# Performance work log

Hardware: AMD Instinct MI355X
Metric: run time of the kernel (lower is better)

## Reference

```python
import jax, jax.numpy as jnp
import numpy as np

B, S, D, DK = 4, 2048, 1024, 1024


def setup_inputs() -> dict:
    key = jax.random.key(0)
    kx, kq, kk, kv = jax.random.split(key, 4)
    return {
        "x": jax.random.normal(kx, (B, S, D), dtype=jnp.float32),
        "WQ": jax.random.normal(kq, (D, DK), dtype=jnp.float32),
        "WK": jax.random.normal(kk, (D, DK), dtype=jnp.float32),
        "WV": jax.random.normal(kv, (D, DK), dtype=jnp.float32),
    }


def reference(x, WQ, WK, WV):
    # q,k,v: [B,S,DK]
    q = x @ WQ
    k = x @ WK
    v = x @ WV
    scale = 1.0 / np.sqrt(DK).astype(np.float32)
    scores = jnp.einsum("bqd,bkd->bqk", q, k) * scale  # [B,S,S]
    # NOTE: original uses nn.Softmax(dim=1) -> normalize over the QUERY axis (axis 1)
    attn = jax.nn.softmax(scores, axis=1)
    return jnp.einsum("bqk,bkd->bqd", attn, v)
```

## Files before the change

kernel.cpp:

```cpp
#include <hip/hip_runtime.h>

constexpr int Bc  = 4;
constexpr int Sc  = 2048;
constexpr int Dc  = 1024;
constexpr int DKc = 1024;
constexpr long BSc = (long)Bc * Sc;

typedef __attribute__((ext_vector_type(8))) __bf16 bf16x8;
typedef __attribute__((ext_vector_type(4))) __bf16 bf16x4;
typedef __attribute__((ext_vector_type(4))) float  floatx4;

__device__ inline __bf16 f2bf(float f) {
  unsigned u = __builtin_bit_cast(unsigned, f);
  u = (u + 0x7FFFu + ((u >> 16) & 1u)) >> 16;
  unsigned short s = (unsigned short)u;
  return __builtin_bit_cast(__bf16, s);
}
__device__ inline float bf2f(__bf16 h) {
  unsigned u = ((unsigned)__builtin_bit_cast(unsigned short, h)) << 16;
  return __builtin_bit_cast(float, u);
}

__device__ inline void stage16(const __bf16* g, __bf16* l) {
  __builtin_amdgcn_global_load_lds(
      (const __attribute__((address_space(1))) unsigned int*)g,
      (__attribute__((address_space(3))) unsigned int*)l, 16, 0, 0);
}

__device__ __forceinline__ void bar_raw() {
  asm volatile("" ::: "memory");
  __builtin_amdgcn_s_barrier();
  asm volatile("" ::: "memory");
}
template <int N>
__device__ __forceinline__ void vmwait() {
  asm volatile("s_waitcnt vmcnt(%0)" :: "n"(N));
  __builtin_amdgcn_sched_barrier(0);
}

__global__ __launch_bounds__(256) void prep(
    const float* __restrict__ x,  __bf16* __restrict__ xhi, __bf16* __restrict__ xlo,
    const float* __restrict__ wq, __bf16* __restrict__ qhi, __bf16* __restrict__ qlo,
    const float* __restrict__ wk, __bf16* __restrict__ khi, __bf16* __restrict__ klo,
    const float* __restrict__ wv, __bf16* __restrict__ vthi) {
  __shared__ float tile[32][33];
  long blk = blockIdx.x;
  if (blk >= 10240) {
    int t   = (int)(blk - 10240);
    int bx  = t & 31, by = t >> 5;
    int thx = threadIdx.x & 31, thy = threadIdx.x >> 5;
    int xI  = bx * 32 + thx, yI = by * 32 + thy;
#pragma unroll
    for (int j = 0; j < 32; j += 8)
      tile[thy + j][thx] = wv[(long)(yI + j) * DKc + xI];
    __syncthreads();
    int xO = by * 32 + thx, yO = bx * 32 + thy;
#pragma unroll
    for (int j = 0; j < 32; j += 8)
      vthi[(long)(yO + j) * Dc + xO] = f2bf(tile[thx][thy + j]);
    return;
  }
  const float* in; __bf16 *hi, *lo; long base;
  if (blk < 8192)      { in = x;  hi = xhi; lo = xlo; base = blk * 1024; }
  else if (blk < 9216) { in = wq; hi = qhi; lo = qlo; base = (blk - 8192) * 1024; }
  else                 { in = wk; hi = khi; lo = klo; base = (blk - 9216) * 1024; }
  long i = base + (long)threadIdx.x * 4;
  float4 f = *(const float4*)(in + i);
  __bf16 h0 = f2bf(f.x), h1 = f2bf(f.y), h2 = f2bf(f.z), h3 = f2bf(f.w);
  bf16x4 hv = {h0, h1, h2, h3};
  bf16x4 lv = {f2bf(f.x - bf2f(h0)), f2bf(f.y - bf2f(h1)),
               f2bf(f.z - bf2f(h2)), f2bf(f.w - bf2f(h3))};
  *(bf16x4*)(hi + i) = hv;
  *(bf16x4*)(lo + i) = lv;
}

struct SCtx {
  const __bf16 *pAh, *pAl, *pBh, *pBl;
  __bf16* lds;
  int stLds;
  int aoff, boff;
};

template <int W, bool SAL, bool S2A, bool S2B>
__device__ __forceinline__ void tile_step(const SCtx& c, int t,
                                          floatx4 (&acc)[8][4]) {
  constexpr int K = 1024;
  constexpr int BH = 8192, BL = 16384, AL = 24576;
  __bf16* cur = c.lds + (t & 1) * 32768;
  __bf16* oth = c.lds + ((t & 1) ^ 1) * 32768;
  bf16x8 af[8], bfr[4], bfl[4];

  vmwait<W>();
  bar_raw();
  if (SAL) {
    const __bf16* s = c.pAl + (t + 1) * 32;
    stage16(s, oth + AL + c.stLds);
    stage16(s + 16 * K, oth + AL + c.stLds + 512);
  }
#pragma unroll
  for (int mt = 0; mt < 8; ++mt)
    af[mt] = *(const bf16x8*)(cur + c.aoff + mt * 512);
#pragma unroll
  for (int nt = 0; nt < 4; ++nt)
    bfr[nt] = *(const bf16x8*)(cur + BH + c.boff + nt * 512);
#pragma unroll
  for (int nt = 0; nt < 4; ++nt)
    bfl[nt] = *(const bf16x8*)(cur + BL + c.boff + nt * 512);

  __builtin_amdgcn_s_setprio(1);
#pragma unroll
  for (int mt = 0; mt < 8; ++mt)
#pragma unroll
    for (int nt = 0; nt < 4; ++nt)
      acc[mt][nt] = __builtin_amdgcn_mfma_f32_16x16x32_bf16(af[mt], bfr[nt], acc[mt][nt], 0, 0, 0);
#pragma unroll
  for (int mt = 0; mt < 8; ++mt)
#pragma unroll
    for (int nt = 0; nt < 4; ++nt)
      acc[mt][nt] = __builtin_amdgcn_mfma_f32_16x16x32_bf16(af[mt], bfl[nt], acc[mt][nt], 0, 0, 0);
  __builtin_amdgcn_s_setprio(0);

  bar_raw();
  if (S2A) {
    const __bf16* sa = c.pAh + (t + 2) * 32;
    stage16(sa, cur + c.stLds);
    stage16(sa + 16 * K, cur + c.stLds + 512);
    stage16(c.pBh + (t + 2) * 32, cur + BH + c.stLds);
  }
  if (S2B) {
    stage16(c.pBh + (t + 2) * 32 + 16 * K, cur + BH + c.stLds + 512);
    const __bf16* sb = c.pBl + (t + 2) * 32;
    stage16(sb, cur + BL + c.stLds);
    stage16(sb + 16 * K, cur + BL + c.stLds + 512);
  }
  {
    bf16x8 afl[8];
#pragma unroll
    for (int mt = 0; mt < 8; ++mt)
      afl[mt] = *(const bf16x8*)(cur + AL + c.aoff + mt * 512);
    __builtin_amdgcn_s_setprio(1);
#pragma unroll
    for (int mt = 0; mt < 8; ++mt)
#pragma unroll
      for (int nt = 0; nt < 4; ++nt)
        acc[mt][nt] = __builtin_amdgcn_mfma_f32_16x16x32_bf16(afl[mt], bfr[nt], acc[mt][nt], 0, 0, 0);
    __builtin_amdgcn_s_setprio(0);
  }
}

__global__ __launch_bounds__(512, 2) void gemm_s5(
    const __bf16* __restrict__ thi, const __bf16* __restrict__ tlo,
    const __bf16* __restrict__ xhi, const __bf16* __restrict__ xlo,
    __bf16* __restrict__ P, float* __restrict__ Pmax, float* __restrict__ Psum) {
  __shared__ __align__(16) __bf16 smem[65536];
  constexpr int K = 1024;
  const int b    = blockIdx.z;
  const int m0   = blockIdx.y * 256;
  const int n0   = blockIdx.x * 256;
  const int wave = threadIdx.x >> 6;
  const int lane = threadIdx.x & 63;
  const int wm   = wave >> 2;
  const int wn   = wave & 3;
  const int sr   = lane >> 2;
  const int scol = ((lane & 3) ^ ((sr >> 1) & 3)) * 8;
  const int frow = lane & 15;
  const int pko  = ((lane >> 4) ^ ((frow >> 1) & 3)) * 8;

  SCtx c;
  const long batch = (long)Sc * 1024;
  const long ar = (long)(m0 + wave * 32 + sr) * K + scol;
  const long br = (long)(n0 + wave * 32 + sr) * K + scol;
  c.pAh = thi + (long)b * batch + ar;
  c.pAl = tlo + (long)b * batch + ar;
  c.pBh = xhi + (long)b * batch + br;
  c.pBl = xlo + (long)b * batch + br;
  c.lds = smem;
  c.stLds = wave * 1024;
  c.aoff = (wm * 128 + frow) * 32 + pko;
  c.boff = (wn * 64 + frow) * 32 + pko;

  {
    __bf16* b0 = smem;
    __bf16* b1 = smem + 32768;
    stage16(c.pAh, b0 + c.stLds);               stage16(c.pAh + 16 * K, b0 + c.stLds + 512);
    stage16(c.pBh, b0 + 8192 + c.stLds);        stage16(c.pBh + 16 * K, b0 + 8192 + c.stLds + 512);
    stage16(c.pBl, b0 + 16384 + c.stLds);       stage16(c.pBl + 16 * K, b0 + 16384 + c.stLds + 512);
    stage16(c.pAl, b0 + 24576 + c.stLds);       stage16(c.pAl + 16 * K, b0 + 24576 + c.stLds + 512);
    stage16(c.pAh + 32, b1 + c.stLds);          stage16(c.pAh + 32 + 16 * K, b1 + c.stLds + 512);
    stage16(c.pBh + 32, b1 + 8192 + c.stLds);   stage16(c.pBh + 32 + 16 * K, b1 + 8192 + c.stLds + 512);
    stage16(c.pBl + 32, b1 + 16384 + c.stLds);  stage16(c.pBl + 32 + 16 * K, b1 + 16384 + c.stLds + 512);
  }

  floatx4 acc[8][4];
  const floatx4 zero = {0.f, 0.f, 0.f, 0.f};
#pragma unroll
  for (int i = 0; i < 8; ++i)
#pragma unroll
    for (int j = 0; j < 4; ++j) acc[i][j] = zero;

#pragma unroll 1
  for (int t = 0; t < 30; ++t) tile_step<6, true, true, true>(c, t, acc);
  tile_step<6, true, false, false>(c, 30, acc);
  tile_step<0, false, false, false>(c, 31, acc);

  const int crow0 = (lane >> 4) * 4;
  const int ccol  = lane & 15;
  const int tid   = threadIdx.x;
  constexpr float scale = 0.03125f;
  float* smax = (float*)smem;
  float* ssum = smax + 512;

  float cm[4];
#pragma unroll
  for (int nt = 0; nt < 4; ++nt) {
    float mx = -3.0e38f;
#pragma unroll
    for (int mt = 0; mt < 8; ++mt)
#pragma unroll
      for (int r = 0; r < 4; ++r) mx = fmaxf(mx, acc[mt][nt][r] * scale);
    cm[nt] = mx;
  }
#pragma unroll
  for (int off = 16; off <= 32; off <<= 1)
#pragma unroll
    for (int nt = 0; nt < 4; ++nt)
      cm[nt] = fmaxf(cm[nt], __shfl_xor(cm[nt], off, 64));
  __syncthreads();
  if (lane < 16)
#pragma unroll
    for (int nt = 0; nt < 4; ++nt)
      smax[wm * 256 + wn * 64 + nt * 16 + lane] = cm[nt];
  __syncthreads();
  float mfin[4];
#pragma unroll
  for (int nt = 0; nt < 4; ++nt) {
    int cidx = wn * 64 + nt * 16 + ccol;
    mfin[nt] = fmaxf(smax[cidx], smax[256 + cidx]);
  }
  float ps[4];
#pragma unroll
  for (int nt = 0; nt < 4; ++nt) {
    float s = 0.f;
#pragma unroll
    for (int mt = 0; mt < 8; ++mt)
#pragma unroll
      for (int r = 0; r < 4; ++r)
        s += __expf(acc[mt][nt][r] * scale - mfin[nt]);
    ps[nt] = s;
  }
#pragma unroll
  for (int off = 16; off <= 32; off <<= 1)
#pragma unroll
    for (int nt = 0; nt < 4; ++nt) ps[nt] += __shfl_xor(ps[nt], off, 64);
  if (lane < 16)
#pragma unroll
    for (int nt = 0; nt < 4; ++nt)
      ssum[wm * 256 + wn * 64 + nt * 16 + lane] = ps[nt];
  __syncthreads();
  if (tid < 256) {
    long o = ((long)b * 8 + blockIdx.y) * Sc + n0 + tid;
    Pmax[o] = fmaxf(smax[tid], smax[256 + tid]);
    Psum[o] = ssum[tid] + ssum[256 + tid];
  }
  __syncthreads();
  __bf16* sT = smem;
#pragma unroll
  for (int nt = 0; nt < 4; ++nt) {
    int col = wn * 64 + nt * 16 + ccol;
#pragma unroll
    for (int mt = 0; mt < 8; ++mt) {
      int rowb = wm * 128 + mt * 16 + crow0;
#pragma unroll
      for (int r = 0; r < 4; ++r) {
        int row = rowb + r;
        sT[row * 256 + (col ^ (((row >> 2) & 3) << 4))] =
            f2bf(__expf(acc[mt][nt][r] * scale - mfin[nt]));
      }
    }
  }
  __syncthreads();
  __bf16* Pb = P + (long)b * ((long)Sc * Sc);
#pragma unroll
  for (int cc = 0; cc < 16; ++cc) {
    int flat = cc * 4096 + tid * 8;
    int row = flat >> 8, col = flat & 255;
    *(bf16x8*)(Pb + (long)(m0 + row) * Sc + n0 + col) =
        *(const bf16x8*)(sT + row * 256 + (col ^ (((row >> 2) & 3) << 4)));
  }
}

struct TCtx {
  const __bf16 *pAh, *pAl, *pBh, *pBl;
  __bf16* lds;
  int stA, stB;
  int aoff, boff;
};

template <int W, bool SAL, bool S2AB, bool S2B>
__device__ __forceinline__ void tile_step_t(const TCtx& c, int t,
                                            floatx4 (&acc)[4][4]) {
  constexpr int K = 1024;
  constexpr int BH = 8192, BL = 12288, AL = 16384, BUF = 24576;
  __bf16* cur = c.lds + (t & 1) * BUF;
  __bf16* oth = c.lds + ((t & 1) ^ 1) * BUF;
  bf16x8 af[4], bfr[4], bfl[4], afl[4];

  vmwait<W>();
  bar_raw();
  if (SAL) {
    const __bf16* s = c.pAl + (t + 1) * 32;
    stage16(s, oth + AL + c.stA);
    stage16(s + 16 * K, oth + AL + c.stA + 512);
  }
#pragma unroll
  for (int mt = 0; mt < 4; ++mt)
    af[mt] = *(const bf16x8*)(cur + c.aoff + mt * 512);
#pragma unroll
  for (int nt = 0; nt < 4; ++nt)
    bfr[nt] = *(const bf16x8*)(cur + BH + c.boff + nt * 512);
#pragma unroll
  for (int nt = 0; nt < 4; ++nt)
    bfl[nt] = *(const bf16x8*)(cur + BL + c.boff + nt * 512);
#pragma unroll
  for (int mt = 0; mt < 4; ++mt)
    afl[mt] = *(const bf16x8*)(cur + AL + c.aoff + mt * 512);

  __builtin_amdgcn_s_setprio(1);
#pragma unroll
  for (int mt = 0; mt < 4; ++mt)
#pragma unroll
    for (int nt = 0; nt < 4; ++nt)
      acc[mt][nt] = __builtin_amdgcn_mfma_f32_16x16x32_bf16(af[mt], bfr[nt], acc[mt][nt], 0, 0, 0);
#pragma unroll
  for (int mt = 0; mt < 4; ++mt)
#pragma unroll
    for (int nt = 0; nt < 4; ++nt)
      acc[mt][nt] = __builtin_amdgcn_mfma_f32_16x16x32_bf16(af[mt], bfl[nt], acc[mt][nt], 0, 0, 0);
#pragma unroll
  for (int mt = 0; mt < 4; ++mt)
#pragma unroll
    for (int nt = 0; nt < 4; ++nt)
      acc[mt][nt] = __builtin_amdgcn_mfma_f32_16x16x32_bf16(afl[mt], bfr[nt], acc[mt][nt], 0, 0, 0);
  __builtin_amdgcn_s_setprio(0);

  bar_raw();
  if (S2AB) {
    const __bf16* sa = c.pAh + (t + 2) * 32;
    stage16(sa, cur + c.stA);
    stage16(sa + 16 * K, cur + c.stA + 512);
    stage16(c.pBh + (t + 2) * 32, cur + BH + c.stB);
  }
  if (S2B) stage16(c.pBl + (t + 2) * 32, cur + BL + c.stB);
}

__global__ __launch_bounds__(512, 2) void gemm_t5(
    const __bf16* __restrict__ xhi, const __bf16* __restrict__ xlo,
    const __bf16* __restrict__ gthi, const __bf16* __restrict__ gtlo,
    __bf16* __restrict__ thi, __bf16* __restrict__ tlo) {
  __shared__ __align__(16) __bf16 smem[49152];
  constexpr int K = 1024;
  const int m0   = blockIdx.y * 256;
  const int n0   = blockIdx.x * 128;
  const int wave = threadIdx.x >> 6;
  const int lane = threadIdx.x & 63;
  const int wm   = wave >> 1;
  const int wn   = wave & 1;
  const int sr   = lane >> 2;
  const int scol = ((lane & 3) ^ ((sr >> 1) & 3)) * 8;
  const int frow = lane & 15;
  const int pko  = ((lane >> 4) ^ ((frow >> 1) & 3)) * 8;

  TCtx c;
  const long ar = (long)(m0 + wave * 32 + sr) * K + scol;
  const long br = (long)(n0 + wave * 16 + sr) * K + scol;
  c.pAh = xhi + ar;
  c.pAl = xlo + ar;
  c.pBh = gthi + br;
  c.pBl = gtlo + br;
  c.lds = smem;
  c.stA = wave * 1024;
  c.stB = wave * 512;
  c.aoff = (wm * 64 + frow) * 32 + pko;
  c.boff = (wn * 64 + frow) * 32 + pko;

  {
    __bf16* b0 = smem;
    __bf16* b1 = smem + 24576;
    stage16(c.pAh, b0 + c.stA);          stage16(c.pAh + 16 * K, b0 + c.stA + 512);
    stage16(c.pBh, b0 + 8192 + c.stB);
    stage16(c.pBl, b0 + 12288 + c.stB);
    stage16(c.pAl, b0 + 16384 + c.stA);  stage16(c.pAl + 16 * K, b0 + 16384 + c.stA + 512);
    stage16(c.pAh + 32, b1 + c.stA);     stage16(c.pAh + 32 + 16 * K, b1 + c.stA + 512);
    stage16(c.pBh + 32, b1 + 8192 + c.stB);
    stage16(c.pBl + 32, b1 + 12288 + c.stB);
  }

  floatx4 acc[4][4];
  const floatx4 zero = {0.f, 0.f, 0.f, 0.f};
#pragma unroll
  for (int i = 0; i < 4; ++i)
#pragma unroll
    for (int j = 0; j < 4; ++j) acc[i][j] = zero;

#pragma unroll 1
  for (int t = 0; t < 30; ++t) tile_step_t<4, true, true, true>(c, t, acc);
  tile_step_t<4, true, false, false>(c, 30, acc);
  tile_step_t<0, false, false, false>(c, 31, acc);

  const int crow0 = (lane >> 4) * 4;
  const int ccol  = lane & 15;
  const int tid   = threadIdx.x;
  __bf16* sT = smem;
#pragma unroll 1
  for (int pass = 0; pass < 2; ++pass) {
    __syncthreads();
#pragma unroll
    for (int nt = 0; nt < 4; ++nt) {
      int col = wn * 64 + nt * 16 + ccol;
#pragma unroll
      for (int mt = 0; mt < 4; ++mt) {
        int rowb = wm * 64 + mt * 16 + crow0;
#pragma unroll
        for (int r = 0; r < 4; ++r) {
          int row = rowb + r;
          float v = acc[mt][nt][r];
          __bf16 h = f2bf(v);
          sT[row * 128 + (col ^ (((row >> 2) & 3) << 4))] =
              pass ? f2bf(v - bf2f(h)) : h;
        }
      }
    }
    __syncthreads();
    __bf16* dst = pass ? tlo : thi;
#pragma unroll
    for (int cc = 0; cc < 8; ++cc) {
      int flat = cc * 4096 + tid * 8;
      int row = flat >> 7, col = flat & 127;
      *(bf16x8*)(dst + (long)(m0 + row) * DKc + n0 + col) =
          *(const bf16x8*)(sT + row * 128 + (col ^ (((row >> 2) & 3) << 4)));
    }
  }
}

struct PCtx {
  const __bf16 *pA, *pB;
  int stA, stB;
  int aoff, boff;
};

template <int KK, int W, bool STG>
__device__ __forceinline__ void tile_step_pv(const PCtx& c, int t,
                                             __bf16* cur, __bf16* dst,
                                             floatx4 (&acc)[4][4]) {
  vmwait<W>();
  bar_raw();
  if (STG) {
    const __bf16* a = c.pA + (t + 2) * 64;
    stage16(a, dst + c.stA);
    stage16(a + 16 * KK, dst + c.stA + 512);
    stage16(c.pB + (t + 2) * 64, dst + 16384 + c.stB);
    stage16(a + 32, dst + 8192 + c.stA);
    stage16(a + 32 + 16 * KK, dst + 8192 + c.stA + 512);
    stage16(c.pB + (t + 2) * 64 + 32, dst + 20480 + c.stB);
  }
  bf16x8 a0[4], b0[4], a1[4], b1[4];
#pragma unroll
  for (int mt = 0; mt < 4; ++mt)
    a0[mt] = *(const bf16x8*)(cur + c.aoff + mt * 512);
#pragma unroll
  for (int nt = 0; nt < 4; ++nt)
    b0[nt] = *(const bf16x8*)(cur + 16384 + c.boff + nt * 512);
#pragma unroll
  for (int mt = 0; mt < 4; ++mt)
    a1[mt] = *(const bf16x8*)(cur + 8192 + c.aoff + mt * 512);
#pragma unroll
  for (int nt = 0; nt < 4; ++nt)
    b1[nt] = *(const bf16x8*)(cur + 20480 + c.boff + nt * 512);
  __builtin_amdgcn_s_setprio(1);
#pragma unroll
  for (int mt = 0; mt < 4; ++mt)
#pragma unroll
    for (int nt = 0; nt < 4; ++nt)
      acc[mt][nt] = __builtin_amdgcn_mfma_f32_16x16x32_bf16(a0[mt], b0[nt], acc[mt][nt], 0, 0, 0);
#pragma unroll
  for (int mt = 0; mt < 4; ++mt)
#pragma unroll
    for (int nt = 0; nt < 4; ++nt)
      acc[mt][nt] = __builtin_amdgcn_mfma_f32_16x16x32_bf16(a1[mt], b1[nt], acc[mt][nt], 0, 0, 0);
  __builtin_amdgcn_s_setprio(0);
}

__global__ __launch_bounds__(256) void scale_p(__bf16* __restrict__ P,
                                               const float* __restrict__ ffac) {
  long i8 = (long)blockIdx.x * 256 + threadIdx.x;
  long base = i8 * 8;
  int k = (int)(base & (Sc - 1));
  int q = (int)((base >> 11) & (Sc - 1));
  int b = (int)(base >> 22);
  int t = q >> 8;
  const float* f = ffac + (((long)b * 8 + t) << 11) + k;
  float4 f0 = *(const float4*)f;
  float4 f1 = *(const float4*)(f + 4);
  bf16x8 p = *(const bf16x8*)(P + base);
  bf16x8 o;
  o[0] = f2bf(bf2f(p[0]) * f0.x);
  o[1] = f2bf(bf2f(p[1]) * f0.y);
  o[2] = f2bf(bf2f(p[2]) * f0.z);
  o[3] = f2bf(bf2f(p[3]) * f0.w);
  o[4] = f2bf(bf2f(p[4]) * f1.x);
  o[5] = f2bf(bf2f(p[5]) * f1.y);
  o[6] = f2bf(bf2f(p[6]) * f1.z);
  o[7] = f2bf(bf2f(p[7]) * f1.w);
  *(bf16x8*)(P + base) = o;
}

__global__ __launch_bounds__(512, 2) void gemm_pv4(
    const __bf16* __restrict__ P, const __bf16* __restrict__ vt,
    float* __restrict__ out) {
  __shared__ __align__(16) __bf16 smem[73728];
  constexpr int K = 2048;
  const int b    = blockIdx.z;
  const int m0   = blockIdx.x * 256;
  const int n0   = blockIdx.y * 128;
  const int wave = threadIdx.x >> 6;
  const int lane = threadIdx.x & 63;
  const int wm   = wave >> 1;
  const int wn   = wave & 1;
  const int sr   = lane >> 2;
  const int scol = ((lane & 3) ^ ((sr >> 1) & 3)) * 8;
  const int frow = lane & 15;
  const int pko  = ((lane >> 4) ^ ((frow >> 1) & 3)) * 8;

  PCtx c;
  c.pA = P + (long)b * Sc * Sc + (long)(m0 + wave * 32 + sr) * K + scol;
  c.pB = vt + (long)b * DKc * Sc + (long)(n0 + wave * 16 + sr) * K + scol;
  c.stA = wave * 1024;
  c.stB = wave * 512;
  c.aoff = (wm * 64 + frow) * 32 + pko;
  c.boff = (wn * 64 + frow) * 32 + pko;

  __bf16* B0 = smem;
  __bf16* B1 = smem + 24576;
  __bf16* B2 = smem + 49152;

  stage16(c.pA, B0 + c.stA);            stage16(c.pA + 16 * K, B0 + c.stA + 512);
  stage16(c.pB, B0 + 16384 + c.stB);
  stage16(c.pA + 32, B0 + 8192 + c.stA); stage16(c.pA + 32 + 16 * K, B0 + 8192 + c.stA + 512);
  stage16(c.pB + 32, B0 + 20480 + c.stB);
  stage16(c.pA + 64, B1 + c.stA);       stage16(c.pA + 64 + 16 * K, B1 + c.stA + 512);
  stage16(c.pB + 64, B1 + 16384 + c.stB);
  stage16(c.pA + 96, B1 + 8192 + c.stA); stage16(c.pA + 96 + 16 * K, B1 + 8192 + c.stA + 512);
  stage16(c.pB + 96, B1 + 20480 + c.stB);

  floatx4 acc[4][4];
  const floatx4 zero = {0.f, 0.f, 0.f, 0.f};
#pragma unroll
  for (int i = 0; i < 4; ++i)
#pragma unroll
    for (int j = 0; j < 4; ++j) acc[i][j] = zero;

#pragma unroll 1
  for (int t = 0; t < 30; t += 3) {
    tile_step_pv<2048, 6, true>(c, t,     B0, B2, acc);
    tile_step_pv<2048, 6, true>(c, t + 1, B1, B0, acc);
    tile_step_pv<2048, 6, true>(c, t + 2, B2, B1, acc);
  }
  tile_step_pv<2048, 6, false>(c, 30, B0, B0, acc);
  tile_step_pv<2048, 0, false>(c, 31, B1, B1, acc);

  const int crow0 = (lane >> 4) * 4;
  const int ccol  = lane & 15;
#pragma unroll
  for (int nt = 0; nt < 4; ++nt) {
    int cn = n0 + wn * 64 + nt * 16 + ccol;
#pragma unroll
    for (int mt = 0; mt < 4; ++mt) {
#pragma unroll
      for (int r = 0; r < 4; ++r) {
        int cm_ = m0 + wm * 64 + mt * 16 + crow0 + r;
        out[(long)b * Sc * DKc + (long)cm_ * DKc + cn] = acc[mt][nt][r];
      }
    }
  }
}

constexpr int VSTR2 = 264;

__global__ __launch_bounds__(512, 2) void gemm_v4(
    const __bf16* __restrict__ xhi, const __bf16* __restrict__ wvthi,
    __bf16* __restrict__ vt) {
  __shared__ __align__(16) __bf16 smem[73728];
  constexpr int K = 1024;
  const int m0   = blockIdx.y * 256;
  const int n0   = blockIdx.x * 128;
  const int wave = threadIdx.x >> 6;
  const int lane = threadIdx.x & 63;
  const int wm   = wave >> 1;
  const int wn   = wave & 1;
  const int sr   = lane >> 2;
  const int scol = ((lane & 3) ^ ((sr >> 1) & 3)) * 8;
  const int frow = lane & 15;
  const int pko  = ((lane >> 4) ^ ((frow >> 1) & 3)) * 8;

  PCtx c;
  c.pA = xhi + (long)(m0 + wave * 32 + sr) * K + scol;
  c.pB = wvthi + (long)(n0 + wave * 16 + sr) * K + scol;
  c.stA = wave * 1024;
  c.stB = wave * 512;
  c.aoff = (wm * 64 + frow) * 32 + pko;
  c.boff = (wn * 64 + frow) * 32 + pko;

  __bf16* B0 = smem;
  __bf16* B1 = smem + 24576;
  __bf16* B2 = smem + 49152;

  stage16(c.pA, B0 + c.stA);            stage16(c.pA + 16 * K, B0 + c.stA + 512);
  stage16(c.pB, B0 + 16384 + c.stB);
  stage16(c.pA + 32, B0 + 8192 + c.stA); stage16(c.pA + 32 + 16 * K, B0 + 8192 + c.stA + 512);
  stage16(c.pB + 32, B0 + 20480 + c.stB);
  stage16(c.pA + 64, B1 + c.stA);       stage16(c.pA + 64 + 16 * K, B1 + c.stA + 512);
  stage16(c.pB + 64, B1 + 16384 + c.stB);
  stage16(c.pA + 96, B1 + 8192 + c.stA); stage16(c.pA + 96 + 16 * K, B1 + 8192 + c.stA + 512);
  stage16(c.pB + 96, B1 + 20480 + c.stB);

  floatx4 acc[4][4];
  const floatx4 zero = {0.f, 0.f, 0.f, 0.f};
#pragma unroll
  for (int i = 0; i < 4; ++i)
#pragma unroll
    for (int j = 0; j < 4; ++j) acc[i][j] = zero;

#pragma unroll 1
  for (int t = 0; t < 12; t += 3) {
    tile_step_pv<1024, 6, true>(c, t,     B0, B2, acc);
    tile_step_pv<1024, 6, true>(c, t + 1, B1, B0, acc);
    tile_step_pv<1024, 6, true>(c, t + 2, B2, B1, acc);
  }
  tile_step_pv<1024, 6, true >(c, 12, B0, B2, acc);
  tile_step_pv<1024, 6, true >(c, 13, B1, B0, acc);
  tile_step_pv<1024, 6, false>(c, 14, B2, B2, acc);
  tile_step_pv<1024, 0, false>(c, 15, B0, B0, acc);

  const int crow0 = (lane >> 4) * 4;
  const int ccol  = lane & 15;
  const int tid   = threadIdx.x;
  __syncthreads();
  __bf16* sT = smem;
#pragma unroll
  for (int nt = 0; nt < 4; ++nt) {
    int nl = wn * 64 + nt * 16 + ccol;
#pragma unroll
    for (int mt = 0; mt < 4; ++mt) {
      int ml = wm * 64 + mt * 16 + crow0;
#pragma unroll
      for (int r = 0; r < 4; ++r)
        sT[(long)nl * VSTR2 + ml + r] = f2bf(acc[mt][nt][r]);
    }
  }
  __syncthreads();
  const int bb   = m0 >> 11;
  const int seq0 = m0 & (Sc - 1);
  __bf16* dst = vt + (long)bb * DKc * Sc + seq0;
#pragma unroll
  for (int cc = 0; cc < 8; ++cc) {
    int flat = cc * 4096 + tid * 8;
    int row = flat >> 8, col = flat & 255;
    *(bf16x8*)(dst + (long)(n0 + row) * Sc + col) =
        *(const bf16x8*)(sT + (long)row * VSTR2 + col);
  }
}

__global__ __launch_bounds__(256) void gemm_g64(
    const __bf16* __restrict__ Ahi, const __bf16* __restrict__ Alo,
    const __bf16* __restrict__ Bhi, const __bf16* __restrict__ Blo,
    __bf16* __restrict__ Chi, __bf16* __restrict__ Clo) {
  constexpr int K = Dc, N = DKc;
  __shared__ __align__(16) char smem[16384];
  __bf16* sAh = (__bf16*)smem;
  __bf16* sBh = sAh + 64 * 32;
  __bf16* sAl = sBh + 64 * 32;
  __bf16* sBl = sAl + 64 * 32;

  const int wave = threadIdx.x >> 6;
  const int lane = threadIdx.x & 63;
  const int wm   = wave >> 1, wn = wave & 1;
  const int m0   = blockIdx.y * 64;
  const int n0   = blockIdx.x * 64;

  const int sr   = lane >> 2;
  const int sc_  = lane & 3;
  const int scol = (sc_ ^ ((sr >> 1) & 3)) * 8;
  const int frow = lane & 15;
  const int pko  = ((lane >> 4) ^ ((frow >> 1) & 3)) * 8;

  floatx4 acc[2][2];
  const floatx4 zero = {0.f, 0.f, 0.f, 0.f};
#pragma unroll
  for (int i = 0; i < 2; ++i)
#pragma unroll
    for (int j = 0; j < 2; ++j) acc[i][j] = zero;

#pragma unroll 1
  for (int k0 = 0; k0 < K; k0 += 32) {
    const int rb = wave * 16;
    const long ga = (long)(m0 + rb + sr) * K + k0 + scol;
    const long gb = (long)(n0 + rb + sr) * K + k0 + scol;
    stage16(Ahi + ga, sAh + rb * 32);
    stage16(Alo + ga, sAl + rb * 32);
    stage16(Bhi + gb, sBh + rb * 32);
    stage16(Blo + gb, sBl + rb * 32);
    __syncthreads();

    bf16x8 af[2], bfr[2], afl[2], bfl[2];
#pragma unroll
    for (int t = 0; t < 2; ++t) {
      af[t]  = *(const bf16x8*)(sAh + (wm * 32 + t * 16 + frow) * 32 + pko);
      bfr[t] = *(const bf16x8*)(sBh + (wn * 32 + t * 16 + frow) * 32 + pko);
      afl[t] = *(const bf16x8*)(sAl + (wm * 32 + t * 16 + frow) * 32 + pko);
      bfl[t] = *(const bf16x8*)(sBl + (wn * 32 + t * 16 + frow) * 32 + pko);
    }
#pragma unroll
    for (int mt = 0; mt < 2; ++mt)
#pragma unroll
      for (int nt = 0; nt < 2; ++nt) {
        acc[mt][nt] = __builtin_amdgcn_mfma_f32_16x16x32_bf16(af[mt], bfr[nt], acc[mt][nt], 0, 0, 0);
        acc[mt][nt] = __builtin_amdgcn_mfma_f32_16x16x32_bf16(af[mt], bfl[nt], acc[mt][nt], 0, 0, 0);
        acc[mt][nt] = __builtin_amdgcn_mfma_f32_16x16x32_bf16(afl[mt], bfr[nt], acc[mt][nt], 0, 0, 0);
      }
    __syncthreads();
  }

  const int crow0 = (lane >> 4) * 4;
  const int ccol  = lane & 15;
  const int tid   = threadIdx.x;
  __bf16* sT = (__bf16*)smem;
#pragma unroll 1
  for (int pass = 0; pass < 2; ++pass) {
    __syncthreads();
#pragma unroll
    for (int nt = 0; nt < 2; ++nt) {
      int col = wn * 32 + nt * 16 + ccol;
#pragma unroll
      for (int mt = 0; mt < 2; ++mt) {
        int row = wm * 32 + mt * 16 + crow0;
#pragma unroll
        for (int r = 0; r < 4; ++r) {
          float v = acc[mt][nt][r];
          __bf16 h = f2bf(v);
          sT[(row + r) * 64 + col] = pass ? f2bf(v - bf2f(h)) : h;
        }
      }
    }
    __syncthreads();
    __bf16* dst = pass ? Clo : Chi;
#pragma unroll
    for (int c = 0; c < 2; ++c) {
      int flat = c * 2048 + tid * 8;
      int row = flat >> 6, col = flat & 63;
      *(bf16x8*)(dst + (long)(m0 + row) * N + n0 + col) = *(const bf16x8*)(sT + flat);
    }
  }
}

__global__ __launch_bounds__(256) void softmax_reduce(const float* __restrict__ Pmax,
                                                      const float* __restrict__ Psum,
                                                      float* __restrict__ Ffac) {
  int idx = blockIdx.x * 256 + threadIdx.x;
  int b = idx >> 11, k = idx & (Sc - 1);
  const float* pm = Pmax + (long)b * 8 * Sc + k;
  const float* ps = Psum + (long)b * 8 * Sc + k;
  float M = -3.0e38f;
#pragma unroll
  for (int t = 0; t < 8; ++t) M = fmaxf(M, pm[(long)t * Sc]);
  float S = 0.f;
#pragma unroll
  for (int t = 0; t < 8; ++t)
    S += ps[(long)t * Sc] * __expf(pm[(long)t * Sc] - M);
  float inv = 1.0f / S;
  float* fo = Ffac + (long)b * 8 * Sc + k;
#pragma unroll
  for (int t = 0; t < 8; ++t)
    fo[(long)t * Sc] = __expf(pm[(long)t * Sc] - M) * inv;
}

extern "C" void kernel_launch(void* const* d_in, const int* in_sizes, int n_in,
                              void* d_out, int out_size, void* d_ws, size_t ws_size,
                              hipStream_t stream) {
  const float* x  = (const float*)d_in[0];
  const float* WQ = (const float*)d_in[1];
  const float* WK = (const float*)d_in[2];
  const float* WV = (const float*)d_in[3];
  float* out = (float*)d_out;
  char* ws = (char*)d_ws;
  const long MB = 1024L * 1024L;

  __bf16* xhi  = (__bf16*)(ws + 0 * MB);
  __bf16* xlo  = (__bf16*)(ws + 16 * MB);
  __bf16* wqhi = (__bf16*)(ws + 32 * MB);
  __bf16* wqlo = (__bf16*)(ws + 34 * MB);
  __bf16* wkhi = (__bf16*)(ws + 36 * MB);
  __bf16* wklo = (__bf16*)(ws + 38 * MB);
  __bf16* wvthi= (__bf16*)(ws + 40 * MB);
  __bf16* gthi = (__bf16*)(ws + 44 * MB);
  __bf16* gtlo = (__bf16*)(ws + 46 * MB);
  __bf16* thi  = (__bf16*)(ws + 48 * MB);
  __bf16* tlo  = (__bf16*)(ws + 64 * MB);
  __bf16* vt   = (__bf16*)(ws + 80 * MB);
  __bf16* P    = (__bf16*)(ws + 96 * MB);
  float*  pmax = (float*)(ws + 128 * MB);
  float*  psum = (float*)(ws + 129 * MB);
  float*  ffac = (float*)(ws + 130 * MB);

  prep<<<11264, 256, 0, stream>>>(x, xhi, xlo, WQ, wqhi, wqlo, WK, wkhi, wklo,
                                  WV, wvthi);

  gemm_g64<<<dim3(16, 16), 256, 0, stream>>>(wkhi, wklo, wqhi, wqlo, gthi, gtlo);

  gemm_t5<<<dim3(DKc / 128, BSc / 256, 1), 512, 0, stream>>>(
      xhi, xlo, gthi, gtlo, thi, tlo);

  gemm_v4<<<dim3(DKc / 128, BSc / 256, 1), 512, 0, stream>>>(xhi, wvthi, vt);

  gemm_s5<<<dim3(Sc / 256, Sc / 256, Bc), 512, 0, stream>>>(
      thi, tlo, xhi, xlo, P, pmax, psum);

  softmax_reduce<<<32, 256, 0, stream>>>(pmax, psum, ffac);

  scale_p<<<8192, 256, 0, stream>>>(P, ffac);

  gemm_pv4<<<dim3(Sc / 256, DKc / 128, Bc), 512, 0, stream>>>(P, vt, out);
}
```

Before: 326.9 us.

## Shrink score GEMM tile to 128x128 with single-buffered LDS

Replaces the 256x256, 512-thread score GEMM with a 128x128, 256-thread version that uses one LDS buffer instead of two. Staging of the next K slice now happens inside the same step behind extra barriers. The softmax partial-statistics layout grows from 8 to 16 row tiles, and the reduce and scale kernels are updated to match. The aim is more blocks and better occupancy. The cost is lower data reuse per block, more global traffic, and load latency that is no longer hidden by double buffering.

```diff
diff --git a/kernel.cpp b/kernel.cpp
--- a/kernel.cpp
+++ b/kernel.cpp
@@ -74,99 +74,99 @@
   *(bf16x4*)(lo + i) = lv;
 }
 
-struct SCtx {
+struct S6Ctx {
   const __bf16 *pAh, *pAl, *pBh, *pBl;
   __bf16* lds;
   int stLds;
   int aoff, boff;
 };
 
-template <int W, bool SAL, bool S2A, bool S2B>
-__device__ __forceinline__ void tile_step(const SCtx& c, int t,
-                                          floatx4 (&acc)[8][4]) {
+template <bool STG, bool STGAL>
+__device__ __forceinline__ void tile_step6(const S6Ctx& c, int t,
+                                           floatx4 (&acc)[4][4]) {
   constexpr int K = 1024;
-  constexpr int BH = 8192, BL = 16384, AL = 24576;
-  __bf16* cur = c.lds + (t & 1) * 32768;
-  __bf16* oth = c.lds + ((t & 1) ^ 1) * 32768;
-  bf16x8 af[8], bfr[4], bfl[4];
-
-  vmwait<W>();
+  constexpr int BH = 4096, BL = 8192, AL = 12288;
+  __bf16* lds = c.lds;
+  bf16x8 af[4], bfr[4], bfl[4];
+
+  vmwait<2>();
   bar_raw();
-  if (SAL) {
-    const __bf16* s = c.pAl + (t + 1) * 32;
-    stage16(s, oth + AL + c.stLds);
-    stage16(s + 16 * K, oth + AL + c.stLds + 512);
-  }
-#pragma unroll
-  for (int mt = 0; mt < 8; ++mt)
-    af[mt] = *(const bf16x8*)(cur + c.aoff + mt * 512);
+#pragma unroll
+  for (int mt = 0; mt < 4; ++mt)
+    af[mt] = *(const bf16x8*)(lds + c.aoff + mt * 512);
 #pragma unroll
   for (int nt = 0; nt < 4; ++nt)
-    bfr[nt] = *(const bf16x8*)(cur + BH + c.boff + nt * 512);
+    bfr[nt] = *(const bf16x8*)(lds + BH + c.boff + nt * 512);
 #pragma unroll
   for (int nt = 0; nt < 4; ++nt)
-    bfl[nt] = *(const bf16x8*)(cur + BL + c.boff + nt * 512);
-
+    bfl[nt] = *(const bf16x8*)(lds + BL + c.boff + nt * 512);
   __builtin_amdgcn_s_setprio(1);
 #pragma unroll
-  for (int mt = 0; mt < 8; ++mt)
+  for (int mt = 0; mt < 4; ++mt)
 #pragma unroll
     for (int nt = 0; nt < 4; ++nt)
       acc[mt][nt] = __builtin_amdgcn_mfma_f32_16x16x32_bf16(af[mt], bfr[nt], acc[mt][nt], 0, 0, 0);
 #pragma unroll
-  for (int mt = 0; mt < 8; ++mt)
+  for (int mt = 0; mt < 4; ++mt)
 #pragma unroll
     for (int nt = 0; nt < 4; ++nt)
       acc[mt][nt] = __builtin_amdgcn_mfma_f32_16x16x32_bf16(af[mt], bfl[nt], acc[mt][nt], 0, 0, 0);
   __builtin_amdgcn_s_setprio(0);
 
+  vmwait<0>();
   bar_raw();
-  if (S2A) {
-    const __bf16* sa = c.pAh + (t + 2) * 32;
-    stage16(sa, cur + c.stLds);
-    stage16(sa + 16 * K, cur + c.stLds + 512);
-    stage16(c.pBh + (t + 2) * 32, cur + BH + c.stLds);
-  }
-  if (S2B) {
-    stage16(c.pBh + (t + 2) * 32 + 16 * K, cur + BH + c.stLds + 512);
-    const __bf16* sb = c.pBl + (t + 2) * 32;
-    stage16(sb, cur + BL + c.stLds);
-    stage16(sb + 16 * K, cur + BL + c.stLds + 512);
+  if (STG) {
+    const __bf16* sa = c.pAh + (t + 1) * 32;
+    stage16(sa, lds + c.stLds);
+    stage16(sa + 16 * K, lds + c.stLds + 512);
+    const __bf16* sb = c.pBh + (t + 1) * 32;
+    stage16(sb, lds + BH + c.stLds);
+    stage16(sb + 16 * K, lds + BH + c.stLds + 512);
+    const __bf16* sl = c.pBl + (t + 1) * 32;
+    stage16(sl, lds + BL + c.stLds);
+    stage16(sl + 16 * K, lds + BL + c.stLds + 512);
   }
   {
-    bf16x8 afl[8];
-#pragma unroll
-    for (int mt = 0; mt < 8; ++mt)
-      afl[mt] = *(const bf16x8*)(cur + AL + c.aoff + mt * 512);
+    bf16x8 afl[4];
+#pragma unroll
+    for (int mt = 0; mt < 4; ++mt)
+      afl[mt] = *(const bf16x8*)(lds + AL + c.aoff + mt * 512);
     __builtin_amdgcn_s_setprio(1);
 #pragma unroll
-    for (int mt = 0; mt < 8; ++mt)
+    for (int mt = 0; mt < 4; ++mt)
 #pragma unroll
       for (int nt = 0; nt < 4; ++nt)
         acc[mt][nt] = __builtin_amdgcn_mfma_f32_16x16x32_bf16(afl[mt], bfr[nt], acc[mt][nt], 0, 0, 0);
     __builtin_amdgcn_s_setprio(0);
   }
-}
-
-__global__ __launch_bounds__(512, 2) void gemm_s5(
+
+  if (STGAL) {
+    bar_raw();
+    const __bf16* s = c.pAl + (t + 1) * 32;
+    stage16(s, lds + AL + c.stLds);
+    stage16(s + 16 * K, lds + AL + c.stLds + 512);
+  }
+}
+
+__global__ __launch_bounds__(256) void gemm_s6(
     const __bf16* __restrict__ thi, const __bf16* __restrict__ tlo,
     const __bf16* __restrict__ xhi, const __bf16* __restrict__ xlo,
     __bf16* __restrict__ P, float* __restrict__ Pmax, float* __restrict__ Psum) {
-  __shared__ __align__(16) __bf16 smem[65536];
+  __shared__ __align__(16) __bf16 smem[16384];
   constexpr int K = 1024;
   const int b    = blockIdx.z;
-  const int m0   = blockIdx.y * 256;
-  const int n0   = blockIdx.x * 256;
+  const int m0   = blockIdx.y * 128;
+  const int n0   = blockIdx.x * 128;
   const int wave = threadIdx.x >> 6;
   const int lane = threadIdx.x & 63;
-  const int wm   = wave >> 2;
-  const int wn   = wave & 3;
+  const int wm   = wave >> 1;
+  const int wn   = wave & 1;
   const int sr   = lane >> 2;
   const int scol = ((lane & 3) ^ ((sr >> 1) & 3)) * 8;
   const int frow = lane & 15;
   const int pko  = ((lane >> 4) ^ ((frow >> 1) & 3)) * 8;
 
-  SCtx c;
+  S6Ctx c;
   const long batch = (long)Sc * 1024;
   const long ar = (long)(m0 + wave * 32 + sr) * K + scol;
   const long br = (long)(n0 + wave * 32 + sr) * K + scol;
@@ -176,46 +176,42 @@
   c.pBl = xlo + (long)b * batch + br;
   c.lds = smem;
   c.stLds = wave * 1024;
-  c.aoff = (wm * 128 + frow) * 32 + pko;
+  c.aoff = (wm * 64 + frow) * 32 + pko;
   c.boff = (wn * 64 + frow) * 32 + pko;
 
-  {
-    __bf16* b0 = smem;
-    __bf16* b1 = smem + 32768;
-    stage16(c.pAh, b0 + c.stLds);               stage16(c.pAh + 16 * K, b0 + c.stLds + 512);
-    stage16(c.pBh, b0 + 8192 + c.stLds);        stage16(c.pBh + 16 * K, b0 + 8192 + c.stLds + 512);
-    stage16(c.pBl, b0 + 16384 + c.stLds);       stage16(c.pBl + 16 * K, b0 + 16384 + c.stLds + 512);
-    stage16(c.pAl, b0 + 24576 + c.stLds);       stage16(c.pAl + 16 * K, b0 + 24576 + c.stLds + 512);
-    stage16(c.pAh + 32, b1 + c.stLds);          stage16(c.pAh + 32 + 16 * K, b1 + c.stLds + 512);
-    stage16(c.pBh + 32, b1 + 8192 + c.stLds);   stage16(c.pBh + 32 + 16 * K, b1 + 8192 + c.stLds + 512);
-    stage16(c.pBl + 32, b1 + 16384 + c.stLds);  stage16(c.pBl + 32 + 16 * K, b1 + 16384 + c.stLds + 512);
-  }
-
-  floatx4 acc[8][4];
+  stage16(c.pAh, smem + c.stLds);
+  stage16(c.pAh + 16 * K, smem + c.stLds + 512);
+  stage16(c.pBh, smem + 4096 + c.stLds);
+  stage16(c.pBh + 16 * K, smem + 4096 + c.stLds + 512);
+  stage16(c.pBl, smem + 8192 + c.stLds);
+  stage16(c.pBl + 16 * K, smem + 8192 + c.stLds + 512);
+  stage16(c.pAl, smem + 12288 + c.stLds);
+  stage16(c.pAl + 16 * K, smem + 12288 + c.stLds + 512);
+
+  floatx4 acc[4][4];
   const floatx4 zero = {0.f, 0.f, 0.f, 0.f};
 #pragma unroll
-  for (int i = 0; i < 8; ++i)
+  for (int i = 0; i < 4; ++i)
 #pragma unroll
     for (int j = 0; j < 4; ++j) acc[i][j] = zero;
 
 #pragma unroll 1
-  for (int t = 0; t < 30; ++t) tile_step<6, true, true, true>(c, t, acc);
-  tile_step<6, true, false, false>(c, 30, acc);
-  tile_step<0, false, false, false>(c, 31, acc);
+  for (int t = 0; t < 31; ++t) tile_step6<true, true>(c, t, acc);
+  tile_step6<false, false>(c, 31, acc);
 
   const int crow0 = (lane >> 4) * 4;
   const int ccol  = lane & 15;
   const int tid   = threadIdx.x;
   constexpr float scale = 0.03125f;
   float* smax = (float*)smem;
-  float* ssum = smax + 512;
+  float* ssum = smax + 256;
 
   float cm[4];
 #pragma unroll
   for (int nt = 0; nt < 4; ++nt) {
     float mx = -3.0e38f;
 #pragma unroll
-    for (int mt = 0; mt < 8; ++mt)
+    for (int mt = 0; mt < 4; ++mt)
 #pragma unroll
       for (int r = 0; r < 4; ++r) mx = fmaxf(mx, acc[mt][nt][r] * scale);
     cm[nt] = mx;
@@ -229,20 +225,20 @@
   if (lane < 16)
 #pragma unroll
     for (int nt = 0; nt < 4; ++nt)
-      smax[wm * 256 + wn * 64 + nt * 16 + lane] = cm[nt];
+      smax[wm * 128 + wn * 64 + nt * 16 + lane] = cm[nt];
   __syncthreads();
   float mfin[4];
 #pragma unroll
   for (int nt = 0; nt < 4; ++nt) {
     int cidx = wn * 64 + nt * 16 + ccol;
-    mfin[nt] = fmaxf(smax[cidx], smax[256 + cidx]);
+    mfin[nt] = fmaxf(smax[cidx], smax[128 + cidx]);
   }
   float ps[4];
 #pragma unroll
   for (int nt = 0; nt < 4; ++nt) {
     float s = 0.f;
 #pragma unroll
-    for (int mt = 0; mt < 8; ++mt)
+    for (int mt = 0; mt < 4; ++mt)
 #pragma unroll
       for (int r = 0; r < 4; ++r)
         s += __expf(acc[mt][nt][r] * scale - mfin[nt]);
@@ -255,12 +251,12 @@
   if (lane < 16)
 #pragma unroll
     for (int nt = 0; nt < 4; ++nt)
-      ssum[wm * 256 + wn * 64 + nt * 16 + lane] = ps[nt];
+      ssum[wm * 128 + wn * 64 + nt * 16 + lane] = ps[nt];
   __syncthreads();
-  if (tid < 256) {
-    long o = ((long)b * 8 + blockIdx.y) * Sc + n0 + tid;
-    Pmax[o] = fmaxf(smax[tid], smax[256 + tid]);
-    Psum[o] = ssum[tid] + ssum[256 + tid];
+  if (tid < 128) {
+    long o = ((long)b * 16 + blockIdx.y) * Sc + n0 + tid;
+    Pmax[o] = fmaxf(smax[tid], smax[128 + tid]);
+    Psum[o] = ssum[tid] + ssum[128 + tid];
   }
   __syncthreads();
   __bf16* sT = smem;
@@ -268,12 +264,12 @@
   for (int nt = 0; nt < 4; ++nt) {
     int col = wn * 64 + nt * 16 + ccol;
 #pragma unroll
-    for (int mt = 0; mt < 8; ++mt) {
-      int rowb = wm * 128 + mt * 16 + crow0;
+    for (int mt = 0; mt < 4; ++mt) {
+      int rowb = wm * 64 + mt * 16 + crow0;
 #pragma unroll
       for (int r = 0; r < 4; ++r) {
         int row = rowb + r;
-        sT[row * 256 + (col ^ (((row >> 2) & 3) << 4))] =
+        sT[row * 128 + (col ^ (((row >> 2) & 3) << 4))] =
             f2bf(__expf(acc[mt][nt][r] * scale - mfin[nt]));
       }
     }
@@ -281,11 +277,11 @@
   __syncthreads();
   __bf16* Pb = P + (long)b * ((long)Sc * Sc);
 #pragma unroll
-  for (int cc = 0; cc < 16; ++cc) {
-    int flat = cc * 4096 + tid * 8;
-    int row = flat >> 8, col = flat & 255;
+  for (int cc = 0; cc < 8; ++cc) {
+    int flat = cc * 2048 + tid * 8;
+    int row = flat >> 7, col = flat & 127;
     *(bf16x8*)(Pb + (long)(m0 + row) * Sc + n0 + col) =
-        *(const bf16x8*)(sT + row * 256 + (col ^ (((row >> 2) & 3) << 4)));
+        *(const bf16x8*)(sT + row * 128 + (col ^ (((row >> 2) & 3) << 4)));
   }
 }
 
@@ -497,8 +493,8 @@
   int k = (int)(base & (Sc - 1));
   int q = (int)((base >> 11) & (Sc - 1));
   int b = (int)(base >> 22);
-  int t = q >> 8;
-  const float* f = ffac + (((long)b * 8 + t) << 11) + k;
+  int t = q >> 7;
+  const float* f = ffac + (((long)b * 16 + t) << 11) + k;
   float4 f0 = *(const float4*)f;
   float4 f1 = *(const float4*)(f + 4);
   bf16x8 p = *(const bf16x8*)(P + base);
@@ -767,19 +763,19 @@
                                                       float* __restrict__ Ffac) {
   int idx = blockIdx.x * 256 + threadIdx.x;
   int b = idx >> 11, k = idx & (Sc - 1);
-  const float* pm = Pmax + (long)b * 8 * Sc + k;
-  const float* ps = Psum + (long)b * 8 * Sc + k;
+  const float* pm = Pmax + (long)b * 16 * Sc + k;
+  const float* ps = Psum + (long)b * 16 * Sc + k;
   float M = -3.0e38f;
 #pragma unroll
-  for (int t = 0; t < 8; ++t) M = fmaxf(M, pm[(long)t * Sc]);
+  for (int t = 0; t < 16; ++t) M = fmaxf(M, pm[(long)t * Sc]);
   float S = 0.f;
 #pragma unroll
-  for (int t = 0; t < 8; ++t)
+  for (int t = 0; t < 16; ++t)
     S += ps[(long)t * Sc] * __expf(pm[(long)t * Sc] - M);
   float inv = 1.0f / S;
-  float* fo = Ffac + (long)b * 8 * Sc + k;
-#pragma unroll
-  for (int t = 0; t < 8; ++t)
+  float* fo = Ffac + (long)b * 16 * Sc + k;
+#pragma unroll
+  for (int t = 0; t < 16; ++t)
     fo[(long)t * Sc] = __expf(pm[(long)t * Sc] - M) * inv;
 }
 
@@ -821,7 +817,7 @@
 
   gemm_v4<<<dim3(DKc / 128, BSc / 256, 1), 512, 0, stream>>>(xhi, wvthi, vt);
 
-  gemm_s5<<<dim3(Sc / 256, Sc / 256, Bc), 512, 0, stream>>>(
+  gemm_s6<<<dim3(Sc / 128, Sc / 128, Bc), 256, 0, stream>>>(
       thi, tlo, xhi, xlo, P, pmax, psum);
 
   softmax_reduce<<<32, 256, 0, stream>>>(pmax, psum, ffac);
```

Measured after the change: 333.5 us. 2.0% more time.
